# Optimization experiments

Measured on AMD Instinct MI355X. Metric: run time of the kernel, lower is better.

The kernel has to match this reference:

```python
import jax, jax.numpy as jnp
import numpy as np

B, MAXLEN, Z, HE, HD, K = 512, 128, 128, 512, 2048, 20
NOUT = 6 * K + 3  # sketch-rnn MDN head: 6 params per mixture + 3 pen logits


def _lstm(x, mask, h0, c0, Wih, Whh, b):
    # x: [B,T,D], mask: [B,T] bool; PyTorch gate order i,f,g,o
    xs = jnp.swapaxes(x, 0, 1)          # [T,B,D]
    ms = jnp.swapaxes(mask, 0, 1)[..., None]  # [T,B,1]

    def step(carry, inp):
        h, c = carry
        xt, mt = inp
        g = xt @ Wih.T + h @ Whh.T + b
        i, f, gg, o = jnp.split(g, 4, axis=-1)
        c2 = jax.nn.sigmoid(f) * c + jax.nn.sigmoid(i) * jnp.tanh(gg)
        h2 = jax.nn.sigmoid(o) * jnp.tanh(c2)
        h2 = jnp.where(mt, h2, h)
        c2 = jnp.where(mt, c2, c)
        return (h2, c2), h2

    (hT, cT), hs = jax.lax.scan(step, (h0, c0), (xs, ms))
    return jnp.swapaxes(hs, 0, 1), hT


def setup_inputs() -> dict:
    key = jax.random.key(0)
    ks = jax.random.split(key, 20)

    def w(k, shape, fan):
        return jax.random.normal(k, shape, jnp.float32) / np.sqrt(fan)

    return {
        "data": jax.random.normal(ks[0], (B, MAXLEN + 1, 2), jnp.float32),
        "eps": jax.random.normal(ks[1], (B, Z), jnp.float32),
        "enc_Wih_f": w(ks[2], (4 * HE, 2), 2),
        "enc_Whh_f": w(ks[3], (4 * HE, HE), HE),
        "enc_b_f": jnp.zeros((4 * HE,), jnp.float32),
        "enc_Wih_b": w(ks[4], (4 * HE, 2), 2),
        "enc_Whh_b": w(ks[5], (4 * HE, HE), HE),
        "enc_b_b": jnp.zeros((4 * HE,), jnp.float32),
        "enc_out_W": 0.001 * jax.random.normal(ks[6], (2 * Z, 2 * HE), jnp.float32),
        "enc_out_b": jnp.zeros((2 * Z,), jnp.float32),
        "init_W": 0.001 * jax.random.normal(ks[7], (2 * HD, Z), jnp.float32),
        "init_b": jnp.zeros((2 * HD,), jnp.float32),
        "dec_Wih": w(ks[8], (4 * HD, 5 + Z), 5 + Z),
        "dec_Whh": w(ks[9], (4 * HD, HD), HD),
        "dec_b": jnp.zeros((4 * HD,), jnp.float32),
        "out_W": w(ks[10], (NOUT, HD), HD),
        "out_b": jnp.zeros((NOUT,), jnp.float32),
        "lengths": jax.random.randint(ks[11], (B,), 1, MAXLEN + 2).astype(jnp.int32),
    }


def reference(data, eps, enc_Wih_f, enc_Whh_f, enc_b_f, enc_Wih_b, enc_Whh_b, enc_b_b,
              enc_out_W, enc_out_b, init_W, init_b, dec_Wih, dec_Whh, dec_b,
              out_W, out_b, lengths):
    enc_in = data[:, 1:MAXLEN + 1, :]   # [B,T,2]
    dec_in = data[:, :MAXLEN, :]        # [B,T,2]

    # --- encoder (bidirectional LSTM with length masking == packed seq) ---
    L = jnp.clip(lengths, 1, MAXLEN)
    t = jnp.arange(MAXLEN)
    mask = t[None, :] < L[:, None]      # [B,T]
    z0 = jnp.zeros((B, HE), jnp.float32)
    _, hF = _lstm(enc_in, mask, z0, z0, enc_Wih_f, enc_Whh_f, enc_b_f)
    # reverse each sequence within its valid length for the backward direction
    idx = jnp.clip(L[:, None] - 1 - t[None, :], 0)
    x_rev = jnp.take_along_axis(enc_in, idx[:, :, None], axis=1)
    _, hB = _lstm(x_rev, mask, z0, z0, enc_Wih_b, enc_Whh_b, enc_b_b)
    h_n = jnp.concatenate([hF, hB], axis=-1)          # [B, 2*HE]
    zm, zl = jnp.split(h_n @ enc_out_W.T + enc_out_b, 2, axis=-1)
    z = zm + jnp.exp(0.5 * zl) * eps                  # reparameterize

    # --- decoder init state ---
    h0, c0 = jnp.split(jnp.tanh(z @ init_W.T + init_b), 2, axis=-1)

    # pad stroke channels 2 -> 5, concat z per step
    dec_pad = jnp.pad(dec_in, ((0, 0), (0, 0), (0, 3)))
    dx = jnp.concatenate(
        [dec_pad, jnp.broadcast_to(z[:, None, :], (B, MAXLEN, Z))], axis=-1)

    full_mask = jnp.ones((B, MAXLEN), bool)
    hs, _ = _lstm(dx, full_mask, h0, c0, dec_Wih, dec_Whh, dec_b)  # [B,T,HD]

    params = hs @ out_W.T + out_b  # [B,T,6K+3] mixture-density params
    return (params, zm, zl)
```

## Files before the change

### kernel.cpp

```cpp
#include <hip/hip_runtime.h>
#include <cstddef>
#include <cstdint>

typedef unsigned short u16;

constexpr int B_ = 512, T_ = 128, Z_ = 128, HE_ = 512, HD_ = 2048, NOUT_ = 123;

constexpr size_t OFF_HF   = 0;
constexpr size_t OFF_CF   = OFF_HF + (size_t)B_*HE_;
constexpr size_t OFF_HB   = OFF_CF + (size_t)B_*HE_;
constexpr size_t OFF_CB   = OFF_HB + (size_t)B_*HE_;
constexpr size_t OFF_HD   = OFF_CB + (size_t)B_*HE_;
constexpr size_t OFF_CD   = OFF_HD + (size_t)B_*HD_;
constexpr size_t OFF_ZW   = OFF_CD + (size_t)B_*HD_;
constexpr size_t OFF_G    = OFF_ZW + (size_t)B_*4*HD_;
constexpr size_t OFF_HN   = OFF_G  + (size_t)B_*4*HD_;
constexpr size_t OFF_ZMZL = OFF_HN + (size_t)B_*2*HE_;
constexpr size_t OFF_Z    = OFF_ZMZL + (size_t)B_*2*Z_;
constexpr size_t OFF_WX   = OFF_Z + (size_t)B_*Z_;
constexpr size_t BASE_FLOATS = OFF_WX + (size_t)2*4*HD_;

constexpr size_t SH_WDEC  = 0;
constexpr size_t SH_WENCF = SH_WDEC  + (size_t)4*HD_*HD_;
constexpr size_t SH_WENCB = SH_WENCF + (size_t)4*HE_*HE_;
constexpr size_t SH_OUTW  = SH_WENCB + (size_t)4*HE_*HE_;
constexpr size_t SH_HDEC  = SH_OUTW  + (size_t)128*HD_;
constexpr size_t SH_HENCF = SH_HDEC  + (size_t)B_*HD_;
constexpr size_t SH_HENCB = SH_HENCF + (size_t)B_*HE_;
constexpr size_t SH_HS    = SH_HENCB + (size_t)B_*HE_;
constexpr size_t HS_SHORTS = (size_t)B_*T_*HD_;

__device__ __forceinline__ float sigm(float x) { return 1.f / (1.f + expf(-x)); }

__device__ __forceinline__ u16 f2bf(float x) {
    union { float f; uint32_t u; } v; v.f = x;
    uint32_t r = v.u + 0x7fffu + ((v.u >> 16) & 1u);
    return (u16)(r >> 16);
}

using bf16x8 = __attribute__((ext_vector_type(8))) short;
using f32x4  = __attribute__((ext_vector_type(4))) float;

__device__ __forceinline__ void gldl16(const void* g, void* l) {
    __builtin_amdgcn_global_load_lds(
        (const __attribute__((address_space(1))) unsigned int*)g,
        (__attribute__((address_space(3))) unsigned int*)l, 16, 0, 0);
}

__global__ __launch_bounds__(256) void gemm_dec64(
    const u16* __restrict__ A, const u16* __restrict__ W, float* __restrict__ C)
{
    __shared__ __align__(16) u16 As[64 * 32];
    __shared__ __align__(16) u16 Ws[128 * 32];
    const int tid = threadIdx.x, lane = tid & 63, wave = tid >> 6;
    const int n0 = blockIdx.x * 128, m0 = blockIdx.y * 64;
    const int wn = wave << 5;
    const int fr = lane & 15, fk = lane >> 4;
    f32x4 acc[4][2] = {};

    const int sr = tid >> 2, sk = (tid & 3) << 3;
    const u16* ga  = A + (size_t)(m0 + sr) * 2048 + sk;
    const u16* gw0 = W + (size_t)(n0 + sr) * 2048 + sk;
    const u16* gw1 = gw0 + (size_t)64 * 2048;
    u16* la  = As + tid * 8;
    u16* lw0 = Ws + tid * 8;
    u16* lw1 = lw0 + 2048;

    for (int k0 = 0; k0 < 2048; k0 += 32) {
        gldl16(ga + k0, la);
        gldl16(gw0 + k0, lw0);
        gldl16(gw1 + k0, lw1);
        __syncthreads();
        bf16x8 af[4], wf[2];
#pragma unroll
        for (int i = 0; i < 4; ++i)
            af[i] = *reinterpret_cast<const bf16x8*>(&As[(i * 16 + fr) * 32 + fk * 8]);
#pragma unroll
        for (int j = 0; j < 2; ++j)
            wf[j] = *reinterpret_cast<const bf16x8*>(&Ws[(wn + j * 16 + fr) * 32 + fk * 8]);
#pragma unroll
        for (int i = 0; i < 4; ++i)
#pragma unroll
            for (int j = 0; j < 2; ++j)
                acc[i][j] = __builtin_amdgcn_mfma_f32_16x16x32_bf16(af[i], wf[j], acc[i][j], 0, 0, 0);
        __syncthreads();
    }

    const int cr = (lane >> 4) << 2, cc = lane & 15;
#pragma unroll
    for (int i = 0; i < 4; ++i) {
#pragma unroll
        for (int j = 0; j < 2; ++j) {
            int n = n0 + wn + j * 16 + cc;
            float* cp = C + (size_t)(m0 + i * 16 + cr) * 8192 + n;
#pragma unroll
            for (int r = 0; r < 4; ++r)
                cp[(size_t)r * 8192] = acc[i][j][r];
        }
    }
}

__device__ __forceinline__ void gemm_mfma_body(
    const u16* __restrict__ A, const u16* __restrict__ W,
    const float* __restrict__ bias, float* __restrict__ C,
    int Kd, int lda, int ldw, int ldc, int nmax, int m0, int n0)
{
    __shared__ __align__(16) u16 As[128 * 32];
    __shared__ __align__(16) u16 Ws[128 * 32];
    const int tid = threadIdx.x;
    const int lane = tid & 63;
    const int wave = tid >> 6;
    const int wm = (wave & 1) << 6, wn = (wave >> 1) << 6;
    const int fr = lane & 15, fk = lane >> 4;
    f32x4 acc[4][4] = {};

    const int sr = tid >> 2, sk = (tid & 3) << 3;
    const u16* ga0 = A + (size_t)(m0 + sr) * lda + sk;
    const u16* ga1 = ga0 + (size_t)64 * lda;
    const u16* gw0 = W + (size_t)(n0 + sr) * ldw + sk;
    const u16* gw1 = gw0 + (size_t)64 * ldw;
    u16* la0 = As + tid * 8;
    u16* la1 = la0 + 2048;
    u16* lw0 = Ws + tid * 8;
    u16* lw1 = lw0 + 2048;

    for (int k0 = 0; k0 < Kd; k0 += 32) {
        gldl16(ga0 + k0, la0);
        gldl16(ga1 + k0, la1);
        gldl16(gw0 + k0, lw0);
        gldl16(gw1 + k0, lw1);
        __syncthreads();
        bf16x8 af[4], wf[4];
#pragma unroll
        for (int i = 0; i < 4; ++i)
            af[i] = *reinterpret_cast<const bf16x8*>(&As[(wm + i * 16 + fr) * 32 + fk * 8]);
#pragma unroll
        for (int j = 0; j < 4; ++j)
            wf[j] = *reinterpret_cast<const bf16x8*>(&Ws[(wn + j * 16 + fr) * 32 + fk * 8]);
#pragma unroll
        for (int i = 0; i < 4; ++i)
#pragma unroll
            for (int j = 0; j < 4; ++j)
                acc[i][j] = __builtin_amdgcn_mfma_f32_16x16x32_bf16(af[i], wf[j], acc[i][j], 0, 0, 0);
        __syncthreads();
    }

    const int cr = (lane >> 4) << 2, cc = lane & 15;
#pragma unroll
    for (int j = 0; j < 4; ++j) {
        int n = n0 + wn + j * 16 + cc;
        if (n < nmax) {
            float bv = bias ? bias[n] : 0.f;
#pragma unroll
            for (int i = 0; i < 4; ++i) {
                int m = m0 + wm + i * 16 + cr;
                float* cp = C + (size_t)m * ldc + n;
#pragma unroll
                for (int r = 0; r < 4; ++r)
                    cp[(size_t)r * ldc] = acc[i][j][r] + bv;
            }
        }
    }
}

__global__ __launch_bounds__(256) void gemm_bf16_k(
    const u16* __restrict__ A, const u16* __restrict__ W,
    const float* __restrict__ bias, float* __restrict__ C,
    int Kd, int lda, int ldw, int ldc, int nmax)
{
    gemm_mfma_body(A, W, bias, C, Kd, lda, ldw, ldc, nmax,
                   blockIdx.x * 128, blockIdx.y * 128);
}

__global__ __launch_bounds__(256) void gemm_enc_mfma(
    const u16* __restrict__ hF, const u16* __restrict__ hB,
    const u16* __restrict__ Wf, const u16* __restrict__ Wb,
    float* __restrict__ g)
{
    const u16* A = blockIdx.z ? hB : hF;
    const u16* W = blockIdx.z ? Wb : Wf;
    float* C = g + (size_t)blockIdx.z * ((size_t)B_ * 4 * HE_);
    gemm_mfma_body(A, W, nullptr, C, HE_, HE_, HE_, 4 * HE_, 4 * HE_,
                   blockIdx.y * 128, blockIdx.x * 128);
}

__device__ __forceinline__ void gemm_body(
    const float* __restrict__ A, const float* __restrict__ W,
    const float* __restrict__ bias, float* __restrict__ C,
    int N, int Kd, int lda, int aoff, int ldw, int woff,
    int ldc, int coff, int m0, int n0)
{
    __shared__ __align__(16) float As[16][68];
    __shared__ __align__(16) float Ws[16][68];
    const int tid = threadIdx.x;
    const int tx = tid & 15, ty = tid >> 4;
    float acc[4][4] = {};
    for (int k0 = 0; k0 < Kd; k0 += 16) {
#pragma unroll
        for (int i = 0; i < 4; ++i) {
            int e = tid + i * 256;
            int mm = e >> 4, kk = e & 15;
            As[kk][mm] = A[(size_t)(m0 + mm) * lda + aoff + k0 + kk];
        }
#pragma unroll
        for (int i = 0; i < 4; ++i) {
            int e = tid + i * 256;
            int nn = e >> 4, kk = e & 15;
            int n = n0 + nn;
            Ws[kk][nn] = (n < N) ? W[(size_t)n * ldw + woff + k0 + kk] : 0.f;
        }
        __syncthreads();
#pragma unroll
        for (int kk = 0; kk < 16; ++kk) {
            float4 a = *reinterpret_cast<const float4*>(&As[kk][ty * 4]);
            float4 w = *reinterpret_cast<const float4*>(&Ws[kk][tx * 4]);
            float av[4] = {a.x, a.y, a.z, a.w};
            float wv[4] = {w.x, w.y, w.z, w.w};
#pragma unroll
            for (int i = 0; i < 4; ++i)
#pragma unroll
                for (int j = 0; j < 4; ++j)
                    acc[i][j] = fmaf(av[i], wv[j], acc[i][j]);
        }
        __syncthreads();
    }
#pragma unroll
    for (int i = 0; i < 4; ++i) {
        int m = m0 + ty * 4 + i;
#pragma unroll
        for (int j = 0; j < 4; ++j) {
            int n = n0 + tx * 4 + j;
            if (n < N) {
                float v = acc[i][j];
                if (bias) v += bias[n];
                C[(size_t)m * ldc + coff + n] = v;
            }
        }
    }
}

__global__ __launch_bounds__(256) void gemm_k(
    const float* __restrict__ A, const float* __restrict__ W,
    const float* __restrict__ bias, float* __restrict__ C,
    int N, int Kd, int lda, int aoff, int ldw, int woff, int ldc, int coff)
{
    gemm_body(A, W, bias, C, N, Kd, lda, aoff, ldw, woff, ldc, coff,
              blockIdx.x * 64, blockIdx.y * 64);
}

__global__ __launch_bounds__(256) void conv_bf16(
    const float* __restrict__ src, u16* __restrict__ dst, int n)
{
    int stride = gridDim.x * 256;
    for (int i = blockIdx.x * 256 + threadIdx.x; i < n; i += stride)
        dst[i] = f2bf(src[i]);
}

__global__ __launch_bounds__(256) void conv_outw(
    const float* __restrict__ w, u16* __restrict__ dst)
{
    int i = blockIdx.x * 256 + threadIdx.x;
    int row = i >> 11, col = i & 2047;
    dst[i] = (row < NOUT_) ? f2bf(w[(size_t)row * HD_ + col]) : (u16)0;
}

__global__ __launch_bounds__(256) void point_enc(
    const float* __restrict__ g, const float* __restrict__ data,
    const float* __restrict__ Wih_f, const float* __restrict__ bf,
    const float* __restrict__ Wih_b, const float* __restrict__ bb,
    const int* __restrict__ lengths,
    float* __restrict__ hF, float* __restrict__ cF,
    float* __restrict__ hB, float* __restrict__ cB,
    u16* __restrict__ hFb, u16* __restrict__ hBb, int t)
{
    int idx = blockIdx.x * 256 + threadIdx.x;
    int dir = idx >> 18;
    int r = idx & ((1 << 18) - 1);
    int b = r >> 9, n = r & 511;
    int L = lengths[b]; L = L < 1 ? 1 : (L > 128 ? 128 : L);
    if (t >= L) return;
    const float* gp = g + (size_t)dir * ((size_t)B_ * 4 * HE_) + (size_t)b * (4 * HE_);
    float gi = gp[n], gf = gp[HE_ + n], gg = gp[2 * HE_ + n], go = gp[3 * HE_ + n];
    int row = dir ? (L - 1 - t) : t;
    float x0 = data[b * 258 + (row + 1) * 2 + 0];
    float x1 = data[b * 258 + (row + 1) * 2 + 1];
    const float* Wih = dir ? Wih_b : Wih_f;
    const float* bias = dir ? bb : bf;
    gi += bias[n]          + x0 * Wih[2 * n]              + x1 * Wih[2 * n + 1];
    gf += bias[HE_ + n]    + x0 * Wih[2 * (HE_ + n)]      + x1 * Wih[2 * (HE_ + n) + 1];
    gg += bias[2*HE_ + n]  + x0 * Wih[2 * (2*HE_ + n)]    + x1 * Wih[2 * (2*HE_ + n) + 1];
    go += bias[3*HE_ + n]  + x0 * Wih[2 * (3*HE_ + n)]    + x1 * Wih[2 * (3*HE_ + n) + 1];
    float* h = dir ? hB : hF;
    float* c = dir ? cB : cF;
    u16* hb = dir ? hBb : hFb;
    int o = b * HE_ + n;
    float c2 = sigm(gf) * c[o] + sigm(gi) * tanhf(gg);
    float h2 = sigm(go) * tanhf(c2);
    h[o] = h2; c[o] = c2; hb[o] = f2bf(h2);
}

__global__ __launch_bounds__(256) void copy_hn(
    const float* __restrict__ hF, const float* __restrict__ hB, float* __restrict__ hn)
{
    int i = blockIdx.x * 256 + threadIdx.x;
    int b = i >> 10, j = i & 1023;
    hn[i] = (j < 512) ? hF[b * 512 + j] : hB[b * 512 + j - 512];
}

__global__ __launch_bounds__(256) void point_z(
    const float* __restrict__ zmzl, const float* __restrict__ eps,
    float* __restrict__ ozm, float* __restrict__ ozl, float* __restrict__ z)
{
    int i = blockIdx.x * 256 + threadIdx.x;
    int b = i >> 7, j = i & 127;
    float zm = zmzl[b * 256 + j], zl = zmzl[b * 256 + 128 + j];
    ozm[i] = zm; ozl[i] = zl;
    z[i] = zm + expf(0.5f * zl) * eps[i];
}

__global__ __launch_bounds__(256) void point_init(
    const float* __restrict__ g, float* __restrict__ h, float* __restrict__ c,
    u16* __restrict__ hb)
{
    int i = blockIdx.x * 256 + threadIdx.x;
    int b = i >> 11, n = i & 2047;
    float hv = tanhf(g[(size_t)b * 4096 + n]);
    h[i] = hv; hb[i] = f2bf(hv);
    c[i] = tanhf(g[(size_t)b * 4096 + 2048 + n]);
}

__global__ __launch_bounds__(256) void prep_wx(
    const float* __restrict__ Wih, float* __restrict__ wx)
{
    int j = blockIdx.x * 256 + threadIdx.x;
    wx[j] = Wih[(size_t)j * 133];
    wx[8192 + j] = Wih[(size_t)j * 133 + 1];
}

__global__ __launch_bounds__(256) void point_dec(
    const float* __restrict__ g, const float* __restrict__ zW,
    const float* __restrict__ data, const float* __restrict__ wx,
    float* __restrict__ h, float* __restrict__ c,
    u16* __restrict__ hb, u16* __restrict__ hs, int t)
{
    int idx = blockIdx.x * 256 + threadIdx.x;
    int b = idx >> 11, n = idx & 2047;
    float x0 = data[b * 258 + t * 2 + 0];
    float x1 = data[b * 258 + t * 2 + 1];
    const float* gp = g + (size_t)b * 8192;
    const float* zp = zW + (size_t)b * 8192;
    int j0 = n, j1 = 2048 + n, j2 = 4096 + n, j3 = 6144 + n;
    float gi = gp[j0] + zp[j0] + x0 * wx[j0] + x1 * wx[8192 + j0];
    float gf = gp[j1] + zp[j1] + x0 * wx[j1] + x1 * wx[8192 + j1];
    float gg = gp[j2] + zp[j2] + x0 * wx[j2] + x1 * wx[8192 + j2];
    float go = gp[j3] + zp[j3] + x0 * wx[j3] + x1 * wx[8192 + j3];
    float c2 = sigm(gf) * c[idx] + sigm(gi) * tanhf(gg);
    float h2 = sigm(go) * tanhf(c2);
    h[idx] = h2; c[idx] = c2;
    u16 hv = f2bf(h2);
    hb[idx] = hv;
    if (hs) hs[(size_t)b * (T_ * HD_) + (size_t)t * HD_ + n] = hv;
}

__global__ __launch_bounds__(256) void proj_step(
    const float* __restrict__ h, const float* __restrict__ out_W,
    const float* __restrict__ out_b, float* __restrict__ out, int t)
{
    __shared__ __align__(16) float sh[2048];
    int b = blockIdx.x;
    for (int i = threadIdx.x; i < 2048; i += 256) sh[i] = h[(size_t)b * 2048 + i];
    __syncthreads();
    int n = threadIdx.x >> 1, half = threadIdx.x & 1;
    if (n >= NOUT_) return;
    const float4* w4 = reinterpret_cast<const float4*>(out_W + (size_t)n * 2048 + half * 1024);
    const float4* h4 = reinterpret_cast<const float4*>(sh + half * 1024);
    float s = 0.f;
#pragma unroll 4
    for (int k = 0; k < 256; ++k) {
        float4 a = h4[k], w = w4[k];
        s += a.x * w.x + a.y * w.y + a.z * w.z + a.w * w.w;
    }
    s += __shfl_xor(s, 1);
    if (half == 0) out[(size_t)b * (T_ * NOUT_) + (size_t)t * NOUT_ + n] = s + out_b[n];
}

extern "C" void kernel_launch(void* const* d_in, const int* in_sizes, int n_in,
                              void* d_out, int out_size, void* d_ws, size_t ws_size,
                              hipStream_t stream)
{
    const float* data      = (const float*)d_in[0];
    const float* eps       = (const float*)d_in[1];
    const float* enc_Wih_f = (const float*)d_in[2];
    const float* enc_Whh_f = (const float*)d_in[3];
    const float* enc_b_f   = (const float*)d_in[4];
    const float* enc_Wih_b = (const float*)d_in[5];
    const float* enc_Whh_b = (const float*)d_in[6];
    const float* enc_b_b   = (const float*)d_in[7];
    const float* enc_out_W = (const float*)d_in[8];
    const float* enc_out_b = (const float*)d_in[9];
    const float* init_W    = (const float*)d_in[10];
    const float* init_b    = (const float*)d_in[11];
    const float* dec_Wih   = (const float*)d_in[12];
    const float* dec_Whh   = (const float*)d_in[13];
    const float* dec_b     = (const float*)d_in[14];
    const float* out_W     = (const float*)d_in[15];
    const float* out_b     = (const float*)d_in[16];
    const int*   lengths   = (const int*)d_in[17];

    float* ws  = (float*)d_ws;
    float* out = (float*)d_out;
    float* hF = ws + OFF_HF, *cF = ws + OFF_CF, *hB = ws + OFF_HB, *cB = ws + OFF_CB;
    float* hd = ws + OFF_HD, *cd = ws + OFF_CD;
    float* zW = ws + OFF_ZW, *g = ws + OFF_G, *hn = ws + OFF_HN;
    float* zmzl = ws + OFF_ZMZL, *z = ws + OFF_Z, *wx = ws + OFF_WX;
    u16* bw = (u16*)(ws + BASE_FLOATS);
    u16* wbDec = bw + SH_WDEC, *wbEncF = bw + SH_WENCF, *wbEncB = bw + SH_WENCB;
    u16* wbOut = bw + SH_OUTW;
    u16* hbDec = bw + SH_HDEC, *hbEncF = bw + SH_HENCF, *hbEncB = bw + SH_HENCB;
    float* ozm = out + (size_t)B_ * T_ * NOUT_;
    float* ozl = ozm + (size_t)B_ * Z_;

    conv_bf16<<<4096, 256, 0, stream>>>(dec_Whh, wbDec, 4 * HD_ * HD_);
    conv_bf16<<<1024, 256, 0, stream>>>(enc_Whh_f, wbEncF, 4 * HE_ * HE_);
    conv_bf16<<<1024, 256, 0, stream>>>(enc_Whh_b, wbEncB, 4 * HE_ * HE_);
    conv_outw<<<1024, 256, 0, stream>>>(out_W, wbOut);

    hipMemsetAsync(ws, 0, (size_t)4 * B_ * HE_ * sizeof(float), stream);
    hipMemsetAsync(hbEncF, 0, (size_t)2 * B_ * HE_ * sizeof(u16), stream);

    for (int t = 0; t < T_; ++t) {
        gemm_enc_mfma<<<dim3(16, 4, 2), 256, 0, stream>>>(hbEncF, hbEncB, wbEncF, wbEncB, g);
        point_enc<<<2048, 256, 0, stream>>>(g, data, enc_Wih_f, enc_b_f, enc_Wih_b, enc_b_b,
                                            lengths, hF, cF, hB, cB, hbEncF, hbEncB, t);
    }

    copy_hn<<<2048, 256, 0, stream>>>(hF, hB, hn);
    gemm_k<<<dim3(8, 4), 256, 0, stream>>>(hn, enc_out_W, enc_out_b, zmzl,
                                           256, 1024, 1024, 0, 1024, 0, 256, 0);
    point_z<<<256, 256, 0, stream>>>(zmzl, eps, ozm, ozl, z);
    gemm_k<<<dim3(8, 64), 256, 0, stream>>>(z, init_W, init_b, g,
                                            4096, 128, 128, 0, 128, 0, 4096, 0);
    point_init<<<4096, 256, 0, stream>>>(g, hd, cd, hbDec);
    gemm_k<<<dim3(8, 128), 256, 0, stream>>>(z, dec_Wih, dec_b, zW,
                                             8192, 128, 128, 0, 133, 5, 8192, 0);
    prep_wx<<<32, 256, 0, stream>>>(dec_Wih, wx);

    bool big = ws_size >= BASE_FLOATS * sizeof(float) + (SH_HS + HS_SHORTS) * sizeof(u16);
    u16* hs = big ? (bw + SH_HS) : nullptr;
    for (int t = 0; t < T_; ++t) {
        gemm_dec64<<<dim3(64, 8), 256, 0, stream>>>(hbDec, wbDec, g);
        point_dec<<<4096, 256, 0, stream>>>(g, zW, data, wx, hd, cd, hbDec, hs, t);
        if (!big) proj_step<<<512, 256, 0, stream>>>(hd, out_W, out_b, out, t);
    }
    if (big) {
        gemm_bf16_k<<<dim3(512, 1), 256, 0, stream>>>(hs, wbOut, out_b, out,
                                                      2048, 2048, 2048, 123, 123);
    }
}
```

Baseline: 15.51 ms.

## Fuse LSTM recurrences into persistent cooperative kernels with gate-interleaved weights

Replaces the per-timestep GEMM plus pointwise kernel launches for the encoder and decoder LSTMs with one persistent cooperative kernel each. Inside, the kernel loops over time with a grid-wide sync per step. Recurrent weights are reordered so the four gates of a hidden unit sit in adjacent columns, which lets the pointwise LSTM update be applied straight from MFMA accumulators via lane shuffles. Cell state stays in registers and hidden state ping-pongs between two bf16 buffers. This removes about 512 kernel launches and the round-trip of fp32 gate tensors through global memory, at the cost of grid.sync overhead and the occupancy limits of a co-resident grid.

```diff
diff --git a/kernel.cpp b/kernel.cpp
--- a/kernel.cpp
+++ b/kernel.cpp
@@ -1,8 +1,10 @@
 #include <hip/hip_runtime.h>
+#include <hip/hip_cooperative_groups.h>
 #include <cstddef>
 #include <cstdint>
 
 typedef unsigned short u16;
+namespace cg = cooperative_groups;
 
 constexpr int B_ = 512, T_ = 128, Z_ = 128, HE_ = 512, HD_ = 2048, NOUT_ = 123;
 
@@ -20,14 +22,17 @@
 constexpr size_t OFF_WX   = OFF_Z + (size_t)B_*Z_;
 constexpr size_t BASE_FLOATS = OFF_WX + (size_t)2*4*HD_;
 
-constexpr size_t SH_WDEC  = 0;
-constexpr size_t SH_WENCF = SH_WDEC  + (size_t)4*HD_*HD_;
-constexpr size_t SH_WENCB = SH_WENCF + (size_t)4*HE_*HE_;
-constexpr size_t SH_OUTW  = SH_WENCB + (size_t)4*HE_*HE_;
-constexpr size_t SH_HDEC  = SH_OUTW  + (size_t)128*HD_;
-constexpr size_t SH_HENCF = SH_HDEC  + (size_t)B_*HD_;
-constexpr size_t SH_HENCB = SH_HENCF + (size_t)B_*HE_;
-constexpr size_t SH_HS    = SH_HENCB + (size_t)B_*HE_;
+constexpr size_t SH_WDEC   = 0;
+constexpr size_t SH_WENCF  = SH_WDEC   + (size_t)4*HD_*HD_;
+constexpr size_t SH_WENCB  = SH_WENCF  + (size_t)4*HE_*HE_;
+constexpr size_t SH_OUTW   = SH_WENCB  + (size_t)4*HE_*HE_;
+constexpr size_t SH_HDEC0  = SH_OUTW   + (size_t)128*HD_;
+constexpr size_t SH_HDEC1  = SH_HDEC0  + (size_t)B_*HD_;
+constexpr size_t SH_HENCF0 = SH_HDEC1  + (size_t)B_*HD_;
+constexpr size_t SH_HENCB0 = SH_HENCF0 + (size_t)B_*HE_;
+constexpr size_t SH_HENCF1 = SH_HENCB0 + (size_t)B_*HE_;
+constexpr size_t SH_HENCB1 = SH_HENCF1 + (size_t)B_*HE_;
+constexpr size_t SH_HS     = SH_HENCB1 + (size_t)B_*HE_;
 constexpr size_t HS_SHORTS = (size_t)B_*T_*HD_;
 
 __device__ __forceinline__ float sigm(float x) { return 1.f / (1.f + expf(-x)); }
@@ -47,56 +52,217 @@
         (__attribute__((address_space(3))) unsigned int*)l, 16, 0, 0);
 }
 
-__global__ __launch_bounds__(256) void gemm_dec64(
-    const u16* __restrict__ A, const u16* __restrict__ W, float* __restrict__ C)
-{
+__global__ __launch_bounds__(256, 2) void dec_persist(
+    const u16* __restrict__ Wil, const float* __restrict__ zwil,
+    const float* __restrict__ wxil, const float* __restrict__ data,
+    const float* __restrict__ c0, u16* __restrict__ h0buf,
+    u16* __restrict__ h1buf, u16* __restrict__ hs)
+{
+    cg::grid_group grd = cg::this_grid();
+    const int nt = blockIdx.x & 63, mt = blockIdx.x >> 6;
+    const int n0 = nt * 128, m0 = mt * 64;
+    const int tid = threadIdx.x, lane = tid & 63, wave = tid >> 6, wn = wave << 5;
+    const int fr = lane & 15, fk = lane >> 4;
+    const int cr = fk << 2, cc = lane & 15;
+    const bool g0 = (lane & 3) == 0;
+    const int lb = lane & ~3;
+
     __shared__ __align__(16) u16 As[64 * 32];
     __shared__ __align__(16) u16 Ws[128 * 32];
-    const int tid = threadIdx.x, lane = tid & 63, wave = tid >> 6;
-    const int n0 = blockIdx.x * 128, m0 = blockIdx.y * 64;
-    const int wn = wave << 5;
-    const int fr = lane & 15, fk = lane >> 4;
-    f32x4 acc[4][2] = {};
-
     const int sr = tid >> 2, sk = (tid & 3) << 3;
-    const u16* ga  = A + (size_t)(m0 + sr) * 2048 + sk;
-    const u16* gw0 = W + (size_t)(n0 + sr) * 2048 + sk;
+    const u16* gw0 = Wil + (size_t)(n0 + sr) * 2048 + sk;
     const u16* gw1 = gw0 + (size_t)64 * 2048;
-    u16* la  = As + tid * 8;
+    u16* la = As + tid * 8;
     u16* lw0 = Ws + tid * 8;
     u16* lw1 = lw0 + 2048;
 
-    for (int k0 = 0; k0 < 2048; k0 += 32) {
-        gldl16(ga + k0, la);
-        gldl16(gw0 + k0, lw0);
-        gldl16(gw1 + k0, lw1);
-        __syncthreads();
-        bf16x8 af[4], wf[2];
+    float c_reg[4][2][4];
+    if (g0) {
 #pragma unroll
         for (int i = 0; i < 4; ++i)
-            af[i] = *reinterpret_cast<const bf16x8*>(&As[(i * 16 + fr) * 32 + fk * 8]);
-#pragma unroll
-        for (int j = 0; j < 2; ++j)
-            wf[j] = *reinterpret_cast<const bf16x8*>(&Ws[(wn + j * 16 + fr) * 32 + fk * 8]);
+#pragma unroll
+            for (int j = 0; j < 2; ++j)
+#pragma unroll
+                for (int r = 0; r < 4; ++r)
+                    c_reg[i][j][r] = c0[(size_t)(m0 + i * 16 + cr + r) * 2048
+                                        + ((n0 + wn + j * 16 + cc) >> 2)];
+    }
+
+    for (int t = 0; t < 128; ++t) {
+        const u16* hin = (t & 1) ? h1buf : h0buf;
+        u16* hout = (t & 1) ? h0buf : h1buf;
+        const u16* ga = hin + (size_t)(m0 + sr) * 2048 + sk;
+        f32x4 acc[4][2] = {};
+        for (int k0 = 0; k0 < 2048; k0 += 32) {
+            gldl16(ga + k0, la);
+            gldl16(gw0 + k0, lw0);
+            gldl16(gw1 + k0, lw1);
+            __syncthreads();
+            bf16x8 af[4], wf[2];
+#pragma unroll
+            for (int i = 0; i < 4; ++i)
+                af[i] = *reinterpret_cast<const bf16x8*>(&As[(i * 16 + fr) * 32 + fk * 8]);
+#pragma unroll
+            for (int j = 0; j < 2; ++j)
+                wf[j] = *reinterpret_cast<const bf16x8*>(&Ws[(wn + j * 16 + fr) * 32 + fk * 8]);
+#pragma unroll
+            for (int i = 0; i < 4; ++i)
+#pragma unroll
+                for (int j = 0; j < 2; ++j)
+                    acc[i][j] = __builtin_amdgcn_mfma_f32_16x16x32_bf16(af[i], wf[j], acc[i][j], 0, 0, 0);
+            __syncthreads();
+        }
+#pragma unroll
+        for (int i = 0; i < 4; ++i) {
+#pragma unroll
+            for (int r = 0; r < 4; ++r) {
+                int m = m0 + i * 16 + cr + r;
+                float x0 = data[m * 258 + t * 2 + 0];
+                float x1 = data[m * 258 + t * 2 + 1];
+#pragma unroll
+                for (int j = 0; j < 2; ++j) {
+                    int np = n0 + wn + j * 16 + cc;
+                    float v = acc[i][j][r] + zwil[(size_t)m * 8192 + np]
+                              + x0 * wxil[np] + x1 * wxil[8192 + np];
+                    float gi = __shfl(v, lb);
+                    float gf = __shfl(v, lb | 1);
+                    float gG = __shfl(v, lb | 2);
+                    float go = __shfl(v, lb | 3);
+                    if (g0) {
+                        float c2 = sigm(gf) * c_reg[i][j][r] + sigm(gi) * tanhf(gG);
+                        float h2 = sigm(go) * tanhf(c2);
+                        c_reg[i][j][r] = c2;
+                        u16 hv = f2bf(h2);
+                        int h = np >> 2;
+                        hout[(size_t)m * 2048 + h] = hv;
+                        hs[(size_t)m * (T_ * HD_) + (size_t)t * HD_ + h] = hv;
+                    }
+                }
+            }
+        }
+        __threadfence();
+        grd.sync();
+    }
+}
+
+__global__ __launch_bounds__(256, 2) void enc_persist(
+    const u16* __restrict__ WF, const u16* __restrict__ WB,
+    const float* __restrict__ ihb,
+    const float* __restrict__ data, const int* __restrict__ lengths,
+    u16* __restrict__ hF0, u16* __restrict__ hF1,
+    u16* __restrict__ hB0, u16* __restrict__ hB1,
+    float* __restrict__ hFout, float* __restrict__ hBout)
+{
+    cg::grid_group grd = cg::this_grid();
+    const int nt = blockIdx.x & 15;
+    const int mt = (blockIdx.x >> 4) & 7;
+    const int dir = blockIdx.x >> 7;
+    const int n0 = nt * 128, m0 = mt * 64;
+    const u16* W = dir ? WB : WF;
+    const float* bIl  = ihb + (size_t)dir * 6144;
+    const float* w0Il = bIl + 2048;
+    const float* w1Il = bIl + 4096;
+    u16* e0 = dir ? hB0 : hF0;
+    u16* e1 = dir ? hB1 : hF1;
+    float* hOut = dir ? hBout : hFout;
+
+    const int tid = threadIdx.x, lane = tid & 63, wave = tid >> 6, wn = wave << 5;
+    const int fr = lane & 15, fk = lane >> 4;
+    const int cr = fk << 2, cc = lane & 15;
+    const bool g0 = (lane & 3) == 0;
+    const int lb = lane & ~3;
+
+    __shared__ __align__(16) u16 As[64 * 32];
+    __shared__ __align__(16) u16 Ws[128 * 32];
+    const int sr = tid >> 2, sk = (tid & 3) << 3;
+    const u16* gw0 = W + (size_t)(n0 + sr) * 512 + sk;
+    const u16* gw1 = gw0 + (size_t)64 * 512;
+    u16* la = As + tid * 8;
+    u16* lw0 = Ws + tid * 8;
+    u16* lw1 = lw0 + 2048;
+
+    int Lr[4][4];
+#pragma unroll
+    for (int i = 0; i < 4; ++i)
+#pragma unroll
+        for (int r = 0; r < 4; ++r) {
+            int L = lengths[m0 + i * 16 + cr + r];
+            Lr[i][r] = L < 1 ? 1 : (L > 128 ? 128 : L);
+        }
+
+    float c_reg[4][2][4] = {};
+    float h_reg[4][2][4] = {};
+
+    for (int t = 0; t < 128; ++t) {
+        const u16* hin = (t & 1) ? e1 : e0;
+        u16* hout = (t & 1) ? e0 : e1;
+        const u16* ga = hin + (size_t)(m0 + sr) * 512 + sk;
+        f32x4 acc[4][2] = {};
+        for (int k0 = 0; k0 < 512; k0 += 32) {
+            gldl16(ga + k0, la);
+            gldl16(gw0 + k0, lw0);
+            gldl16(gw1 + k0, lw1);
+            __syncthreads();
+            bf16x8 af[4], wf[2];
+#pragma unroll
+            for (int i = 0; i < 4; ++i)
+                af[i] = *reinterpret_cast<const bf16x8*>(&As[(i * 16 + fr) * 32 + fk * 8]);
+#pragma unroll
+            for (int j = 0; j < 2; ++j)
+                wf[j] = *reinterpret_cast<const bf16x8*>(&Ws[(wn + j * 16 + fr) * 32 + fk * 8]);
+#pragma unroll
+            for (int i = 0; i < 4; ++i)
+#pragma unroll
+                for (int j = 0; j < 2; ++j)
+                    acc[i][j] = __builtin_amdgcn_mfma_f32_16x16x32_bf16(af[i], wf[j], acc[i][j], 0, 0, 0);
+            __syncthreads();
+        }
+#pragma unroll
+        for (int i = 0; i < 4; ++i) {
+#pragma unroll
+            for (int r = 0; r < 4; ++r) {
+                int m = m0 + i * 16 + cr + r;
+                int L = Lr[i][r];
+                bool act = t < L;
+                int row = dir ? (L - 1 - t) : t;
+                if (row < 0) row = 0;
+                float x0 = data[m * 258 + (row + 1) * 2 + 0];
+                float x1 = data[m * 258 + (row + 1) * 2 + 1];
+#pragma unroll
+                for (int j = 0; j < 2; ++j) {
+                    int np = n0 + wn + j * 16 + cc;
+                    float v = acc[i][j][r] + bIl[np] + x0 * w0Il[np] + x1 * w1Il[np];
+                    float gi = __shfl(v, lb);
+                    float gf = __shfl(v, lb | 1);
+                    float gG = __shfl(v, lb | 2);
+                    float go = __shfl(v, lb | 3);
+                    if (g0) {
+                        if (act) {
+                            float c2 = sigm(gf) * c_reg[i][j][r] + sigm(gi) * tanhf(gG);
+                            float h2 = sigm(go) * tanhf(c2);
+                            c_reg[i][j][r] = c2;
+                            h_reg[i][j][r] = h2;
+                        }
+                        hout[(size_t)m * 512 + (np >> 2)] = f2bf(h_reg[i][j][r]);
+                    }
+                }
+            }
+        }
+        __threadfence();
+        grd.sync();
+    }
+    if (g0) {
 #pragma unroll
         for (int i = 0; i < 4; ++i)
 #pragma unroll
-            for (int j = 0; j < 2; ++j)
-                acc[i][j] = __builtin_amdgcn_mfma_f32_16x16x32_bf16(af[i], wf[j], acc[i][j], 0, 0, 0);
-        __syncthreads();
-    }
-
-    const int cr = (lane >> 4) << 2, cc = lane & 15;
-#pragma unroll
-    for (int i = 0; i < 4; ++i) {
-#pragma unroll
-        for (int j = 0; j < 2; ++j) {
-            int n = n0 + wn + j * 16 + cc;
-            float* cp = C + (size_t)(m0 + i * 16 + cr) * 8192 + n;
-#pragma unroll
-            for (int r = 0; r < 4; ++r)
-                cp[(size_t)r * 8192] = acc[i][j][r];
-        }
+            for (int r = 0; r < 4; ++r) {
+                int m = m0 + i * 16 + cr + r;
+#pragma unroll
+                for (int j = 0; j < 2; ++j) {
+                    int np = n0 + wn + j * 16 + cc;
+                    hOut[(size_t)m * 512 + (np >> 2)] = h_reg[i][j][r];
+                }
+            }
     }
 }
 
@@ -184,6 +350,55 @@
                    blockIdx.y * 128, blockIdx.x * 128);
 }
 
+__global__ __launch_bounds__(256) void gemm_dec64(
+    const u16* __restrict__ A, const u16* __restrict__ W, float* __restrict__ C)
+{
+    __shared__ __align__(16) u16 As[64 * 32];
+    __shared__ __align__(16) u16 Ws[128 * 32];
+    const int tid = threadIdx.x, lane = tid & 63, wave = tid >> 6;
+    const int n0 = blockIdx.x * 128, m0 = blockIdx.y * 64;
+    const int wn = wave << 5;
+    const int fr = lane & 15, fk = lane >> 4;
+    f32x4 acc[4][2] = {};
+    const int sr = tid >> 2, sk = (tid & 3) << 3;
+    const u16* ga  = A + (size_t)(m0 + sr) * 2048 + sk;
+    const u16* gw0 = W + (size_t)(n0 + sr) * 2048 + sk;
+    const u16* gw1 = gw0 + (size_t)64 * 2048;
+    u16* la  = As + tid * 8;
+    u16* lw0 = Ws + tid * 8;
+    u16* lw1 = lw0 + 2048;
+    for (int k0 = 0; k0 < 2048; k0 += 32) {
+        gldl16(ga + k0, la);
+        gldl16(gw0 + k0, lw0);
+        gldl16(gw1 + k0, lw1);
+        __syncthreads();
+        bf16x8 af[4], wf[2];
+#pragma unroll
+        for (int i = 0; i < 4; ++i)
+            af[i] = *reinterpret_cast<const bf16x8*>(&As[(i * 16 + fr) * 32 + fk * 8]);
+#pragma unroll
+        for (int j = 0; j < 2; ++j)
+            wf[j] = *reinterpret_cast<const bf16x8*>(&Ws[(wn + j * 16 + fr) * 32 + fk * 8]);
+#pragma unroll
+        for (int i = 0; i < 4; ++i)
+#pragma unroll
+            for (int j = 0; j < 2; ++j)
+                acc[i][j] = __builtin_amdgcn_mfma_f32_16x16x32_bf16(af[i], wf[j], acc[i][j], 0, 0, 0);
+        __syncthreads();
+    }
+    const int cr = (lane >> 4) << 2, cc = lane & 15;
+#pragma unroll
+    for (int i = 0; i < 4; ++i)
+#pragma unroll
+        for (int j = 0; j < 2; ++j) {
+            int n = n0 + wn + j * 16 + cc;
+            float* cp = C + (size_t)(m0 + i * 16 + cr) * 8192 + n;
+#pragma unroll
+            for (int r = 0; r < 4; ++r)
+                cp[(size_t)r * 8192] = acc[i][j][r];
+        }
+}
+
 __device__ __forceinline__ void gemm_body(
     const float* __restrict__ A, const float* __restrict__ W,
     const float* __restrict__ bias, float* __restrict__ C,
@@ -256,12 +471,81 @@
         dst[i] = f2bf(src[i]);
 }
 
+__global__ __launch_bounds__(256) void conv_wdec_il(
+    const float* __restrict__ src, u16* __restrict__ dst)
+{
+    int row = blockIdx.x;
+    int g = row >> 11, h = row & 2047;
+    size_t so = (size_t)row * 2048, dofs = (size_t)(h * 4 + g) * 2048;
+    for (int k = threadIdx.x; k < 2048; k += 256)
+        dst[dofs + k] = f2bf(src[so + k]);
+}
+
+__global__ __launch_bounds__(256) void conv_wenc_il(
+    const float* __restrict__ srcF, const float* __restrict__ srcB,
+    u16* __restrict__ dstF, u16* __restrict__ dstB)
+{
+    int row = blockIdx.x & 2047;
+    int dir = blockIdx.x >> 11;
+    const float* s = dir ? srcB : srcF;
+    u16* d = dir ? dstB : dstF;
+    int g = row >> 9, h = row & 511;
+    size_t so = (size_t)row * 512, dofs = (size_t)(h * 4 + g) * 512;
+    for (int k = threadIdx.x; k < 512; k += 256)
+        d[dofs + k] = f2bf(s[so + k]);
+}
+
 __global__ __launch_bounds__(256) void conv_outw(
     const float* __restrict__ w, u16* __restrict__ dst)
 {
     int i = blockIdx.x * 256 + threadIdx.x;
     int row = i >> 11, col = i & 2047;
     dst[i] = (row < NOUT_) ? f2bf(w[(size_t)row * HD_ + col]) : (u16)0;
+}
+
+__global__ __launch_bounds__(256) void prep_enc_ihb(
+    const float* __restrict__ WihF, const float* __restrict__ bF,
+    const float* __restrict__ WihB, const float* __restrict__ bB,
+    float* __restrict__ ihb)
+{
+    int i = blockIdx.x * 256 + threadIdx.x;
+    if (i >= 4096) return;
+    int dir = i >> 11, np = i & 2047;
+    int gate = np & 3, h = np >> 2;
+    int no = gate * 512 + h;
+    const float* Wih = dir ? WihB : WihF;
+    const float* b = dir ? bB : bF;
+    float* o = ihb + (size_t)dir * 6144;
+    o[np] = b[no];
+    o[2048 + np] = Wih[2 * no];
+    o[4096 + np] = Wih[2 * no + 1];
+}
+
+__global__ __launch_bounds__(256) void zw_il(
+    const float* __restrict__ zw, float* __restrict__ zwil)
+{
+    int i = blockIdx.x * 256 + threadIdx.x;
+    int m = i >> 13, np = i & 8191;
+    int gate = np & 3, h = np >> 2;
+    zwil[i] = zw[(size_t)m * 8192 + gate * 2048 + h];
+}
+
+__global__ __launch_bounds__(256) void prep_wx_il(
+    const float* __restrict__ Wih, float* __restrict__ wxil)
+{
+    int np = blockIdx.x * 256 + threadIdx.x;
+    int gate = np & 3, h = np >> 2;
+    size_t row = (size_t)(gate * 2048 + h) * 133;
+    wxil[np] = Wih[row];
+    wxil[8192 + np] = Wih[row + 1];
+}
+
+__global__ __launch_bounds__(256) void prep_wx(
+    const float* __restrict__ Wih, float* __restrict__ wx)
+{
+    int j = blockIdx.x * 256 + threadIdx.x;
+    wx[j] = Wih[(size_t)j * 133];
+    wx[8192 + j] = Wih[(size_t)j * 133 + 1];
 }
 
 __global__ __launch_bounds__(256) void point_enc(
@@ -329,14 +613,6 @@
     c[i] = tanhf(g[(size_t)b * 4096 + 2048 + n]);
 }
 
-__global__ __launch_bounds__(256) void prep_wx(
-    const float* __restrict__ Wih, float* __restrict__ wx)
-{
-    int j = blockIdx.x * 256 + threadIdx.x;
-    wx[j] = Wih[(size_t)j * 133];
-    wx[8192 + j] = Wih[(size_t)j * 133 + 1];
-}
-
 __global__ __launch_bounds__(256) void point_dec(
     const float* __restrict__ g, const float* __restrict__ zW,
     const float* __restrict__ data, const float* __restrict__ wx,
@@ -413,47 +689,87 @@
     float* hd = ws + OFF_HD, *cd = ws + OFF_CD;
     float* zW = ws + OFF_ZW, *g = ws + OFF_G, *hn = ws + OFF_HN;
     float* zmzl = ws + OFF_ZMZL, *z = ws + OFF_Z, *wx = ws + OFF_WX;
+    float* zwil = g;
+    float* ihb  = hn;
     u16* bw = (u16*)(ws + BASE_FLOATS);
-    u16* wbDec = bw + SH_WDEC, *wbEncF = bw + SH_WENCF, *wbEncB = bw + SH_WENCB;
-    u16* wbOut = bw + SH_OUTW;
-    u16* hbDec = bw + SH_HDEC, *hbEncF = bw + SH_HENCF, *hbEncB = bw + SH_HENCB;
+    u16* wbDec  = bw + SH_WDEC, *wbEncF = bw + SH_WENCF, *wbEncB = bw + SH_WENCB;
+    u16* wbOut  = bw + SH_OUTW;
+    u16* hD0 = bw + SH_HDEC0, *hD1 = bw + SH_HDEC1;
+    u16* hEF0 = bw + SH_HENCF0, *hEB0 = bw + SH_HENCB0;
+    u16* hEF1 = bw + SH_HENCF1, *hEB1 = bw + SH_HENCB1;
+    u16* hs = bw + SH_HS;
     float* ozm = out + (size_t)B_ * T_ * NOUT_;
     float* ozl = ozm + (size_t)B_ * Z_;
 
-    conv_bf16<<<4096, 256, 0, stream>>>(dec_Whh, wbDec, 4 * HD_ * HD_);
-    conv_bf16<<<1024, 256, 0, stream>>>(enc_Whh_f, wbEncF, 4 * HE_ * HE_);
-    conv_bf16<<<1024, 256, 0, stream>>>(enc_Whh_b, wbEncB, 4 * HE_ * HE_);
-    conv_outw<<<1024, 256, 0, stream>>>(out_W, wbOut);
-
-    hipMemsetAsync(ws, 0, (size_t)4 * B_ * HE_ * sizeof(float), stream);
-    hipMemsetAsync(hbEncF, 0, (size_t)2 * B_ * HE_ * sizeof(u16), stream);
-
-    for (int t = 0; t < T_; ++t) {
-        gemm_enc_mfma<<<dim3(16, 4, 2), 256, 0, stream>>>(hbEncF, hbEncB, wbEncF, wbEncB, g);
-        point_enc<<<2048, 256, 0, stream>>>(g, data, enc_Wih_f, enc_b_f, enc_Wih_b, enc_b_b,
-                                            lengths, hF, cF, hB, cB, hbEncF, hbEncB, t);
-    }
-
-    copy_hn<<<2048, 256, 0, stream>>>(hF, hB, hn);
-    gemm_k<<<dim3(8, 4), 256, 0, stream>>>(hn, enc_out_W, enc_out_b, zmzl,
-                                           256, 1024, 1024, 0, 1024, 0, 256, 0);
-    point_z<<<256, 256, 0, stream>>>(zmzl, eps, ozm, ozl, z);
-    gemm_k<<<dim3(8, 64), 256, 0, stream>>>(z, init_W, init_b, g,
-                                            4096, 128, 128, 0, 128, 0, 4096, 0);
-    point_init<<<4096, 256, 0, stream>>>(g, hd, cd, hbDec);
-    gemm_k<<<dim3(8, 128), 256, 0, stream>>>(z, dec_Wih, dec_b, zW,
-                                             8192, 128, 128, 0, 133, 5, 8192, 0);
-    prep_wx<<<32, 256, 0, stream>>>(dec_Wih, wx);
-
     bool big = ws_size >= BASE_FLOATS * sizeof(float) + (SH_HS + HS_SHORTS) * sizeof(u16);
-    u16* hs = big ? (bw + SH_HS) : nullptr;
-    for (int t = 0; t < T_; ++t) {
-        gemm_dec64<<<dim3(64, 8), 256, 0, stream>>>(hbDec, wbDec, g);
-        point_dec<<<4096, 256, 0, stream>>>(g, zW, data, wx, hd, cd, hbDec, hs, t);
-        if (!big) proj_step<<<512, 256, 0, stream>>>(hd, out_W, out_b, out, t);
-    }
-    if (big) {
+    int occD = 0, occE = 0;
+    hipOccupancyMaxActiveBlocksPerMultiprocessor(&occD, dec_persist, 256, 0);
+    hipOccupancyMaxActiveBlocksPerMultiprocessor(&occE, enc_persist, 256, 0);
+    bool use_p = big && occD >= 2 && occE >= 1;
+
+    if (use_p) {
+        conv_wdec_il<<<8192, 256, 0, stream>>>(dec_Whh, wbDec);
+        conv_wenc_il<<<4096, 256, 0, stream>>>(enc_Whh_f, enc_Whh_b, wbEncF, wbEncB);
+        conv_outw<<<1024, 256, 0, stream>>>(out_W, wbOut);
+        prep_enc_ihb<<<16, 256, 0, stream>>>(enc_Wih_f, enc_b_f, enc_Wih_b, enc_b_b, ihb);
+        hipMemsetAsync(hEF0, 0, (size_t)2 * B_ * HE_ * sizeof(u16), stream);
+
+        void* ea[] = { (void*)&wbEncF, (void*)&wbEncB, (void*)&ihb, (void*)&data,
+                       (void*)&lengths, (void*)&hEF0, (void*)&hEF1, (void*)&hEB0,
+                       (void*)&hEB1, (void*)&hF, (void*)&hB };
+        hipLaunchCooperativeKernel(enc_persist, dim3(256), dim3(256), ea, 0, stream);
+
+        copy_hn<<<2048, 256, 0, stream>>>(hF, hB, hn);
+        gemm_k<<<dim3(8, 4), 256, 0, stream>>>(hn, enc_out_W, enc_out_b, zmzl,
+                                               256, 1024, 1024, 0, 1024, 0, 256, 0);
+        point_z<<<256, 256, 0, stream>>>(zmzl, eps, ozm, ozl, z);
+        gemm_k<<<dim3(8, 64), 256, 0, stream>>>(z, init_W, init_b, zW,
+                                                4096, 128, 128, 0, 128, 0, 4096, 0);
+        point_init<<<4096, 256, 0, stream>>>(zW, hd, cd, hD0);
+        gemm_k<<<dim3(8, 128), 256, 0, stream>>>(z, dec_Wih, dec_b, zW,
+                                                 8192, 128, 128, 0, 133, 5, 8192, 0);
+        zw_il<<<16384, 256, 0, stream>>>(zW, zwil);
+        prep_wx_il<<<32, 256, 0, stream>>>(dec_Wih, ws + OFF_WX);
+
+        void* da[] = { (void*)&wbDec, (void*)&zwil, (void*)&wx, (void*)&data,
+                       (void*)&cd, (void*)&hD0, (void*)&hD1, (void*)&hs };
+        hipLaunchCooperativeKernel(dec_persist, dim3(512), dim3(256), da, 0, stream);
+
         gemm_bf16_k<<<dim3(512, 1), 256, 0, stream>>>(hs, wbOut, out_b, out,
                                                       2048, 2048, 2048, 123, 123);
-    }
-}
+    } else {
+        conv_bf16<<<4096, 256, 0, stream>>>(dec_Whh, wbDec, 4 * HD_ * HD_);
+        conv_bf16<<<1024, 256, 0, stream>>>(enc_Whh_f, wbEncF, 4 * HE_ * HE_);
+        conv_bf16<<<1024, 256, 0, stream>>>(enc_Whh_b, wbEncB, 4 * HE_ * HE_);
+        conv_outw<<<1024, 256, 0, stream>>>(out_W, wbOut);
+        hipMemsetAsync(ws, 0, (size_t)4 * B_ * HE_ * sizeof(float), stream);
+        hipMemsetAsync(hEF0, 0, (size_t)2 * B_ * HE_ * sizeof(u16), stream);
+
+        for (int t = 0; t < T_; ++t) {
+            gemm_enc_mfma<<<dim3(16, 4, 2), 256, 0, stream>>>(hEF0, hEB0, wbEncF, wbEncB, g);
+            point_enc<<<2048, 256, 0, stream>>>(g, data, enc_Wih_f, enc_b_f, enc_Wih_b, enc_b_b,
+                                                lengths, hF, cF, hB, cB, hEF0, hEB0, t);
+        }
+        copy_hn<<<2048, 256, 0, stream>>>(hF, hB, hn);
+        gemm_k<<<dim3(8, 4), 256, 0, stream>>>(hn, enc_out_W, enc_out_b, zmzl,
+                                               256, 1024, 1024, 0, 1024, 0, 256, 0);
+        point_z<<<256, 256, 0, stream>>>(zmzl, eps, ozm, ozl, z);
+        gemm_k<<<dim3(8, 64), 256, 0, stream>>>(z, init_W, init_b, g,
+                                                4096, 128, 128, 0, 128, 0, 4096, 0);
+        point_init<<<4096, 256, 0, stream>>>(g, hd, cd, hD0);
+        gemm_k<<<dim3(8, 128), 256, 0, stream>>>(z, dec_Wih, dec_b, zW,
+                                                 8192, 128, 128, 0, 133, 5, 8192, 0);
+        prep_wx<<<32, 256, 0, stream>>>(dec_Wih, wx);
+
+        u16* hsf = big ? hs : nullptr;
+        for (int t = 0; t < T_; ++t) {
+            gemm_dec64<<<dim3(64, 8), 256, 0, stream>>>(hD0, wbDec, g);
+            point_dec<<<4096, 256, 0, stream>>>(g, zW, data, wx, hd, cd, hD0, hsf, t);
+            if (!big) proj_step<<<512, 256, 0, stream>>>(hd, out_W, out_b, out, t);
+        }
+        if (big) {
+            gemm_bf16_k<<<dim3(512, 1), 256, 0, stream>>>(hs, wbOut, out_b, out,
+                                                          2048, 2048, 2048, 123, 123);
+        }
+    }
+}
```

Result: no change. 15.43 ms (-0.5%).
